# Performance work log

Measured on AMD Instinct MI355X. Metric: run time of the kernel, lower is better.

The kernel has to match this reference:

```python
import jax, jax.numpy as jnp
import numpy as np

L = 2        # NUM_DECODER_LAYERS
D = 512      # D_MODEL == ENCODER_EMBEDDING_DIM == DECODER_EMBEDDING_DIM == DECODER_HIDDEN_DIM
T = 32       # max_trg_len (greedy decode steps)
SOS = 1      # SPECIAL_TOKENS.index('[SOS]'), PAD assumed 0


def setup_inputs() -> dict:
    key = jax.random.key(0)
    ks = jax.random.split(key, 12)
    Vin, Vout, B, S = 32000, 32000, 32, 512
    s = 0.02
    src = jax.random.randint(ks[0], (B, S), 0, Vin)
    src_emb_table = jax.random.normal(ks[1], (Vin, D), dtype=jnp.float32) * s
    trg_emb_table = (jax.random.normal(ks[2], (Vout, D), dtype=jnp.float32) * s).at[0].set(0.0)  # padding_idx=0
    Wih = jax.random.normal(ks[3], (L, 4 * D, D), dtype=jnp.float32) * s
    Whh = jax.random.normal(ks[4], (L, 4 * D, D), dtype=jnp.float32) * s
    bih = jnp.zeros((L, 4 * D), jnp.float32)
    bhh = jnp.zeros((L, 4 * D), jnp.float32)
    Wfc = jax.random.normal(ks[5], (D, D), dtype=jnp.float32) * s      # Decoder.fc_out (hid_dim -> hid_dim)
    bfc = jnp.zeros((D,), jnp.float32)
    Wh2o = jax.random.normal(ks[6], (D, 2 * D), dtype=jnp.float32) * s  # hidden_to_out
    bh2o = jnp.zeros((D,), jnp.float32)
    bout = jnp.zeros((Vout,), jnp.float32)                              # out_layer bias (weight tied to trg_emb_table)
    return dict(src=src, src_emb_table=src_emb_table, trg_emb_table=trg_emb_table,
                Wih=Wih, Whh=Whh, bih=bih, bhh=bhh, Wfc=Wfc, bfc=bfc,
                Wh2o=Wh2o, bh2o=bh2o, bout=bout)


def reference(src, src_emb_table, trg_emb_table, Wih, Whh, bih, bhh, Wfc, bfc, Wh2o, bh2o, bout):
    B, S = src.shape
    dtype = src_emb_table.dtype
    scale = jnp.asarray(D ** 0.5, dtype)
    src_e = src_emb_table[src]  # [B,S,D] -- encoder LSTM hidden/cell are computed but discarded in the original

    def lstm_cell(x, h, c, l):
        g = x @ Wih[l].T + bih[l] + h @ Whh[l].T + bhh[l]
        i, f, gg, o = jnp.split(g, 4, axis=-1)  # torch gate order i,f,g,o
        c2 = jax.nn.sigmoid(f) * c + jax.nn.sigmoid(i) * jnp.tanh(gg)
        h2 = jax.nn.sigmoid(o) * jnp.tanh(c2)
        return h2, c2

    def outer_step(carry, t):
        # Original re-runs the decoder LSTM over the whole generated prefix every
        # step, starting from the carried hidden state; we mask positions > t.
        tokens, h, c = carry  # tokens [B,T+1] int32, h/c [L,B,D]
        emb = jnp.swapaxes(trg_emb_table[tokens[:, :T]], 0, 1)  # [T,B,D]

        def pos_step(hc, inp):
            h, c = hc
            x, pos = inp
            active = pos <= t
            hs, cs = [], []
            for l in range(L):
                h2, c2 = lstm_cell(x, h[l], c[l], l)
                h2 = jnp.where(active, h2, h[l])
                c2 = jnp.where(active, c2, c[l])
                hs.append(h2); cs.append(c2)
                x = h2
            h, c = jnp.stack(hs), jnp.stack(cs)
            return (h, c), h[-1]

        (h, c), h_top = jax.lax.scan(pos_step, (h, c), (emb, jnp.arange(T)))
        out_seq = h_top @ Wfc.T + bfc                 # [T,B,D] Decoder.fc_out
        out_t = jnp.take(out_seq, t, axis=0)          # last valid position (concat[:, -1])
        w = jax.nn.softmax(jnp.einsum('bd,bsd->bs', out_t, src_e) / scale, axis=-1)
        context = jnp.einsum('bs,bsd->bd', w, src_e)
        hid = jax.nn.relu(jnp.concatenate([out_t, context], axis=-1) @ Wh2o.T + bh2o)
        logits = hid @ trg_emb_table.T + bout         # out_layer tied to decoder embedding
        nxt = jnp.argmax(logits, axis=-1).astype(tokens.dtype)
        tokens = tokens.at[:, t + 1].set(nxt)
        return (tokens, h, c), out_seq

    tokens0 = jnp.zeros((B, T + 1), jnp.int32).at[:, 0].set(SOS)
    h0 = jnp.zeros((L, B, D), dtype)
    (tokens, _, _), out_seqs = jax.lax.scan(outer_step, (tokens0, h0, h0), jnp.arange(T))
    # attn returned by the original is from the LAST decode step, queries = all T positions
    attn = jax.nn.softmax(jnp.einsum('tbd,bsd->bts', out_seqs[-1], src_e) / scale, axis=-1)  # [B,T,S]
    return tokens[:, 1:], attn
```

## Files before the change

### kernel.cpp

```cpp
#include <hip/hip_runtime.h>
#include <math.h>

#define NWG 256
#define TPB 512
#define AGT __HIP_MEMORY_SCOPE_AGENT

static constexpr int Bb = 32, Dd = 512, Tt = 32, Vv = 32000;
static constexpr int BD = Bb * Dd;
static constexpr float SCALE_INV = 0.04419417382415922f;

static constexpr size_t OFF_H0 = 8192;
static constexpr size_t OFF_H1 = OFF_H0 + 2 * (size_t)BD;
static constexpr size_t OFF_P  = OFF_H1 + 2 * (size_t)BD;
static constexpr size_t OFF_HL = OFF_P + (size_t)Tt * Bb * 2048;
static constexpr size_t OFF_HD = OFF_HL + (size_t)Tt * BD;
static constexpr size_t OFF_OF = OFF_HD + BD;
static constexpr size_t OFF_CV = OFF_OF + (size_t)Tt * BD;
static constexpr size_t OFF_CI = OFF_CV + 32 * 256;
static constexpr size_t OFF_ET = OFF_CI + 32 * 256;

static constexpr int L_W   = 0;
static constexpr int L_ST  = 13824;
static constexpr int L_SC  = 13824;
static constexpr int L_RB  = 14336;
static constexpr int L_IB  = 15360;
static constexpr int L_RED = 15872;
static constexpr int L_HB  = 30208;
static constexpr int L_GV  = 32256;
static constexpr int L_GI  = 32512;
static constexpr int L_TOK = 32768;
static constexpr int LDS_FLOATS = 32800;
static constexpr size_t LDS_BYTES = (size_t)LDS_FLOATS * 4;

__device__ __forceinline__ float sigm(float x) { return 1.0f / (1.0f + expf(-x)); }

__device__ __forceinline__ float ldcv(const float* p) {
  unsigned u = __hip_atomic_load((const unsigned*)p, __ATOMIC_RELAXED, AGT);
  return __builtin_bit_cast(float, u);
}
__device__ __forceinline__ void stcv(float* p, float v) {
  __hip_atomic_store((unsigned*)p, __builtin_bit_cast(unsigned, v), __ATOMIC_RELAXED, AGT);
}
__device__ __forceinline__ float2 ldcv2(const float* p) {
  unsigned long long u = __hip_atomic_load((const unsigned long long*)p, __ATOMIC_RELAXED, AGT);
  return __builtin_bit_cast(float2, u);
}
__device__ __forceinline__ void stcv2(float* p, float2 v) {
  __hip_atomic_store((unsigned long long*)p, __builtin_bit_cast(unsigned long long, v),
                     __ATOMIC_RELAXED, AGT);
}
__device__ __forceinline__ int ldcvi(const int* p) {
  return (int)__hip_atomic_load((const unsigned*)p, __ATOMIC_RELAXED, AGT);
}
__device__ __forceinline__ void stcvi(int* p, int v) {
  __hip_atomic_store((unsigned*)p, (unsigned)v, __ATOMIC_RELAXED, AGT);
}

__device__ __forceinline__ float wredsum(float v) {
#pragma unroll
  for (int off = 32; off > 0; off >>= 1) v += __shfl_xor(v, off, 64);
  return v;
}

__device__ __forceinline__ float rowReduce16(float x) {
  int t;
  t = __builtin_amdgcn_update_dpp(0, __builtin_bit_cast(int, x), 0x121, 0xF, 0xF, false);
  x += __builtin_bit_cast(float, t);
  t = __builtin_amdgcn_update_dpp(0, __builtin_bit_cast(int, x), 0x122, 0xF, 0xF, false);
  x += __builtin_bit_cast(float, t);
  t = __builtin_amdgcn_update_dpp(0, __builtin_bit_cast(int, x), 0x124, 0xF, 0xF, false);
  x += __builtin_bit_cast(float, t);
  t = __builtin_amdgcn_update_dpp(0, __builtin_bit_cast(int, x), 0x128, 0xF, 0xF, false);
  x += __builtin_bit_cast(float, t);
  return x;
}

__device__ __forceinline__ int swzH(int byte) { return byte ^ (((byte >> 8) & 7) << 4); }

__device__ __forceinline__ void gbar(unsigned* sb, unsigned& lg) {
  const unsigned tgt = lg + 1u;
  asm volatile("s_waitcnt vmcnt(0)" ::: "memory");
  __syncthreads();
  const int wg = (int)blockIdx.x;
  if (threadIdx.x < 64) {
    const int lane = (int)threadIdx.x;
    if (lane == 0)
      __hip_atomic_store(&sb[wg * 16], tgt, __ATOMIC_RELAXED, AGT);
    const int g = wg >> 5;
    if ((wg & 31) == 0) {
      if (lane < 32) {
        const unsigned* slot = &sb[(g * 32 + lane) * 16];
        while (__hip_atomic_load(slot, __ATOMIC_RELAXED, AGT) < tgt)
          __builtin_amdgcn_s_sleep(1);
      }
      if (lane == 0)
        __hip_atomic_store(&sb[4096 + g * 16], tgt, __ATOMIC_RELAXED, AGT);
    }
    if (lane < 8) {
      const unsigned* f = &sb[4096 + lane * 16];
      while (__hip_atomic_load(f, __ATOMIC_RELAXED, AGT) < tgt)
        __builtin_amdgcn_s_sleep(1);
    }
  }
  lg = tgt;
  __syncthreads();
}

__device__ __forceinline__ float blockMax(float v, float* red, int tid) {
#pragma unroll
  for (int off = 32; off > 0; off >>= 1) v = fmaxf(v, __shfl_xor(v, off, 64));
  if ((tid & 63) == 0) red[tid >> 6] = v;
  __syncthreads();
  float m = red[0];
#pragma unroll
  for (int i = 1; i < 8; ++i) m = fmaxf(m, red[i]);
  __syncthreads();
  return m;
}

__device__ __forceinline__ float blockSum(float v, float* red, int tid) {
  v = wredsum(v);
  if ((tid & 63) == 0) red[tid >> 6] = v;
  __syncthreads();
  float s = 0.f;
#pragma unroll
  for (int i = 0; i < 8; ++i) s += red[i];
  __syncthreads();
  return s;
}

__device__ void stageW(int wg, int tid, const float* __restrict__ Wih,
                       const float* __restrict__ Whh, float* __restrict__ SMW) {
  for (int e = tid; e < 24 * 512; e += TPB) {
    const int k = e & 511, rr = e >> 9;
    const int m = rr >> 3, q = (rr >> 1) & 3, dl = rr & 1;
    const int j = q * 512 + wg * 2 + dl;
    const float* srcp = (m == 0) ? (Whh + (size_t)j * 512)
                     : (m == 1) ? (Wih + (size_t)2048 * 512 + (size_t)j * 512)
                                : (Whh + (size_t)2048 * 512 + (size_t)j * 512);
    SMW[rr * 576 + (k >> 5) * 36 + (k & 31)] = srcp[k];
  }
  __syncthreads();
}

__device__ void buildETb(int wg, int tid, const float* __restrict__ Etrg,
                         float* __restrict__ ETb, float* __restrict__ SM) {
  if (wg < 250) {
    for (int tile = 0; tile < 8; ++tile) {
      const int tv = tile >> 2, tk = tile & 3;
      __syncthreads();
      for (int e = tid; e < 64 * 128; e += TPB) {
        const int vl = e >> 7, kl = e & 127;
        SM[vl * 129 + kl] = Etrg[(size_t)(wg * 128 + tv * 64 + vl) * 512 + tk * 128 + kl];
      }
      __syncthreads();
      for (int e = tid; e < 32 * 128; e += TPB) {
        const int vp = e >> 7, kl = e & 127;
        const int v = wg * 128 + tv * 64 + vp * 2;
        const int k = tk * 128 + kl;
        float2 val = make_float2(SM[(vp * 2) * 129 + kl], SM[(vp * 2 + 1) * 129 + kl]);
        stcv2(ETb + ((size_t)(v >> 1) * 512 + k) * 2, val);
      }
    }
    __syncthreads();
  }
}

__device__ __forceinline__ void dotMQ(const float* __restrict__ SMW, int rr, int kc,
                                      const float4* __restrict__ hq, float2& acc) {
  const float4* wr = (const float4*)(SMW + rr * 576 + kc * 36);
#pragma unroll
  for (int i2 = 0; i2 < 8; ++i2) {
    const float4 wv = wr[i2];
    const float4 hA = hq[i2 * 2], hB = hq[i2 * 2 + 1];
    acc.x = fmaf(wv.x, hA.x, acc.x); acc.y = fmaf(wv.x, hA.y, acc.y);
    acc.x = fmaf(wv.y, hA.z, acc.x); acc.y = fmaf(wv.y, hA.w, acc.y);
    acc.x = fmaf(wv.z, hB.x, acc.x); acc.y = fmaf(wv.z, hB.y, acc.y);
    acc.x = fmaf(wv.w, hB.z, acc.x); acc.y = fmaf(wv.w, hB.w, acc.y);
  }
}

__device__ __forceinline__ void phaseAB(
    int wg, int tid, bool doA, bool doB,
    const float* __restrict__ H0r, float* __restrict__ H0w,
    const float* __restrict__ H1r, float* __restrict__ H1w,
    float* __restrict__ HlP, const float* __restrict__ Pp,
    const float* __restrict__ bs1v,
    const float* __restrict__ SMW, float* __restrict__ LH, float* c0, float* c1)
{
  const int b2 = tid >> 5, dl = (tid >> 4) & 1, kc = tid & 15;
  char* LHc = (char*)LH;
  float4 s0[8], s1[8];
  __builtin_amdgcn_sched_barrier(0);
  {
    const float* p0 = H0r + tid * 4;
#pragma unroll
    for (int r = 0; r < 8; ++r)
      asm volatile("global_load_dwordx4 %0, %1, off sc1" : "=v"(s0[r]) : "v"(p0 + r * 2048));
  }
  if (doB) {
    const float* p1 = H1r + tid * 4;
#pragma unroll
    for (int r = 0; r < 8; ++r)
      asm volatile("global_load_dwordx4 %0, %1, off sc1" : "=v"(s1[r]) : "v"(p1 + r * 2048));
    asm volatile("s_waitcnt vmcnt(8)" ::: "memory");
  } else {
    asm volatile("s_waitcnt vmcnt(0)" ::: "memory");
  }
  __builtin_amdgcn_sched_barrier(0);
#pragma unroll
  for (int r = 0; r < 8; ++r)
    *(float4*)(LHc + swzH((r * 512 + tid) * 16)) = s0[r];
  __syncthreads();
  float4 hq[16];
#pragma unroll
  for (int i = 0; i < 16; ++i)
    hq[i] = *(const float4*)(LHc + swzH(b2 * 4096 + kc * 256 + i * 16));

  float2 acc2[12];
#pragma unroll
  for (int j = 0; j < 12; ++j) acc2[j] = make_float2(0.f, 0.f);

  if (doA) {
#pragma unroll
    for (int q = 0; q < 4; ++q) dotMQ(SMW, q * 2 + dl, kc, hq, acc2[q]);
  }
  if (doB) {
#pragma unroll
    for (int q = 0; q < 4; ++q) dotMQ(SMW, 8 + q * 2 + dl, kc, hq, acc2[4 + q]);
    asm volatile("s_waitcnt vmcnt(0)" ::: "memory");
    __builtin_amdgcn_sched_barrier(0);
    __syncthreads();
#pragma unroll
    for (int r = 0; r < 8; ++r)
      *(float4*)(LHc + swzH((r * 512 + tid) * 16)) = s1[r];
    __syncthreads();
#pragma unroll
    for (int i = 0; i < 16; ++i)
      hq[i] = *(const float4*)(LHc + swzH(b2 * 4096 + kc * 256 + i * 16));
#pragma unroll
    for (int q = 0; q < 4; ++q) dotMQ(SMW, 16 + q * 2 + dl, kc, hq, acc2[8 + q]);
  }

#pragma unroll
  for (int j = 0; j < 12; ++j) {
    if (j < 4 ? !doA : !doB) continue;
    acc2[j].x = rowReduce16(acc2[j].x);
    acc2[j].y = rowReduce16(acc2[j].y);
  }

  if (kc == 0) {
    const int d = (wg << 1) | dl;
    if (doA) {
#pragma unroll
      for (int p = 0; p < 2; ++p) {
        const int b = b2 * 2 + p;
        const float* pb = Pp + b * 2048 + d;
        const float gi = (p ? acc2[0].y : acc2[0].x) + pb[0];
        const float gf = (p ? acc2[1].y : acc2[1].x) + pb[512];
        const float gg = (p ? acc2[2].y : acc2[2].x) + pb[1024];
        const float go = (p ? acc2[3].y : acc2[3].x) + pb[1536];
        c0[p] = sigm(gf) * c0[p] + sigm(gi) * tanhf(gg);
        stcv(H0w + b2 * 1024 + d * 2 + p, sigm(go) * tanhf(c0[p]));
      }
    }
    if (doB) {
#pragma unroll
      for (int p = 0; p < 2; ++p) {
        const float gi = (p ? acc2[4].y : acc2[4].x) + (p ? acc2[8].y  : acc2[8].x)  + bs1v[0];
        const float gf = (p ? acc2[5].y : acc2[5].x) + (p ? acc2[9].y  : acc2[9].x)  + bs1v[1];
        const float gg = (p ? acc2[6].y : acc2[6].x) + (p ? acc2[10].y : acc2[10].x) + bs1v[2];
        const float go = (p ? acc2[7].y : acc2[7].x) + (p ? acc2[11].y : acc2[11].x) + bs1v[3];
        c1[p] = sigm(gf) * c1[p] + sigm(gi) * tanhf(gg);
        const float hn = sigm(go) * tanhf(c1[p]);
        stcv(H1w + b2 * 1024 + d * 2 + p, hn);
        if (HlP) stcv(HlP + b2 * 1024 + d * 2 + p, hn);
      }
    }
  }
}

__device__ void phaseCDEF(int b, int tid, const float* __restrict__ H1c,
                          const float* __restrict__ Wfc, const float* __restrict__ bfc,
                          const int* __restrict__ src, const float* __restrict__ Esrc,
                          const float* __restrict__ Wh2o, const float* __restrict__ bh2o,
                          float* __restrict__ hD, float* sc, float* rb, int* ib, float* red)
{
  rb[tid] = ldcv(H1c + (b >> 1) * 1024 + tid * 2 + (b & 1));
  ib[tid] = src[b * 512 + tid];
  __syncthreads();
  const int w = tid >> 6, lane = tid & 63;
  for (int d = w; d < 512; d += 8) {
    const float* wr = Wfc + (size_t)d * 512;
    float p = 0.f;
#pragma unroll
    for (int i = 0; i < 8; ++i) p = fmaf(rb[lane * 8 + i], wr[lane * 8 + i], p);
    p = wredsum(p);
    if (lane == 0) rb[512 + d] = p + bfc[d];
  }
  __syncthreads();
  for (int s = w; s < 512; s += 8) {
    const float* er = Esrc + (size_t)ib[s] * 512;
    float p = 0.f;
#pragma unroll
    for (int i = 0; i < 8; ++i) p = fmaf(rb[512 + lane * 8 + i], er[lane * 8 + i], p);
    p = wredsum(p);
    if (lane == 0) sc[s] = p * SCALE_INV;
  }
  __syncthreads();
  const float mx = blockMax(sc[tid], red, tid);
  const float e = expf(sc[tid] - mx);
  sc[tid] = e;
  const float sum = blockSum(e, red, tid);
  const float inv = 1.0f / sum;
  float acc = 0.f;
#pragma unroll 4
  for (int s = 0; s < 512; ++s) acc = fmaf(sc[s], Esrc[(size_t)ib[s] * 512 + tid], acc);
  rb[tid] = acc * inv;
  __syncthreads();
  for (int d = w; d < 512; d += 8) {
    const float* wr = Wh2o + (size_t)d * 1024;
    float p = 0.f;
#pragma unroll
    for (int i = 0; i < 8; ++i) p = fmaf(rb[512 + lane * 8 + i], wr[lane * 8 + i], p);
#pragma unroll
    for (int i = 0; i < 8; ++i) p = fmaf(rb[lane * 8 + i], wr[512 + lane * 8 + i], p);
    p = wredsum(p);
    if (lane == 0) stcv(hD + (size_t)b * 512 + d, fmaxf(p + bh2o[d], 0.f));
  }
}

__device__ void phaseG(int wg, int tid, int chunk, float* __restrict__ accG,
                       const float* __restrict__ hD, const float* __restrict__ ETb,
                       const float* __restrict__ bout, float* __restrict__ candV,
                       int* __restrict__ candI, float* __restrict__ hblk,
                       float* __restrict__ gv, int* __restrict__ gi)
{
  if (wg >= 250) return;
  if (chunk == 0) {
#pragma unroll
    for (int j = 0; j < 8; ++j) accG[j] = 0.f;
  }
  const int vp = tid >> 3, bh = tid & 7;
  const int v = wg * 128 + vp * 2;
  const float* ep = ETb + (size_t)(v >> 1) * 1024 + chunk * 512;
  const int fk = tid & 63, fb0 = tid >> 6;
  char* hb = (char*)hblk;

  for (int blk = 0; blk < 4; ++blk) {
    const int kb = chunk * 256 + blk * 64;
    __syncthreads();
#pragma unroll
    for (int i = 0; i < 4; ++i) {
      const int b = fb0 + i * 8;
      const float hv = ldcv(hD + (size_t)b * 512 + kb + fk);
      const int byte = fk * 128 + (((b >> 2) * 16) ^ ((fk & 7) << 4)) + ((b & 3) << 2);
      *(float*)(hb + byte) = hv;
    }
    __syncthreads();
#pragma unroll 8
    for (int kk = 0; kk < 64; kk += 2) {
      const float4 e4 = *(const float4*)ep; ep += 4;
      const float4 ha = *(const float4*)(hb + kk * 128 + ((bh * 16) ^ ((kk & 7) << 4)));
      const float4 hbv = *(const float4*)(hb + (kk + 1) * 128 + ((bh * 16) ^ (((kk + 1) & 7) << 4)));
      accG[0] = fmaf(e4.x, ha.x, accG[0]);  accG[4] = fmaf(e4.y, ha.x, accG[4]);
      accG[1] = fmaf(e4.x, ha.y, accG[1]);  accG[5] = fmaf(e4.y, ha.y, accG[5]);
      accG[2] = fmaf(e4.x, ha.z, accG[2]);  accG[6] = fmaf(e4.y, ha.z, accG[6]);
      accG[3] = fmaf(e4.x, ha.w, accG[3]);  accG[7] = fmaf(e4.y, ha.w, accG[7]);
      accG[0] = fmaf(e4.z, hbv.x, accG[0]); accG[4] = fmaf(e4.w, hbv.x, accG[4]);
      accG[1] = fmaf(e4.z, hbv.y, accG[1]); accG[5] = fmaf(e4.w, hbv.y, accG[5]);
      accG[2] = fmaf(e4.z, hbv.z, accG[2]); accG[6] = fmaf(e4.w, hbv.z, accG[6]);
      accG[3] = fmaf(e4.z, hbv.w, accG[3]); accG[7] = fmaf(e4.w, hbv.w, accG[7]);
    }
  }

  if (chunk == 1) {
    const float bo0 = bout[v], bo1 = bout[v + 1];
    const int w = tid >> 6;
#pragma unroll
    for (int j = 0; j < 4; ++j) {
      const float va = accG[j] + bo0, vb = accG[4 + j] + bo1;
      float bv; int bi;
      if (vb > va) { bv = vb; bi = v + 1; } else { bv = va; bi = v; }
#pragma unroll
      for (int off = 8; off < 64; off <<= 1) {
        const float ov = __shfl_xor(bv, off, 64); const int oi = __shfl_xor(bi, off, 64);
        if (ov > bv || (ov == bv && oi < bi)) { bv = ov; bi = oi; }
      }
      if ((tid & 63) < 8) {
        gv[(bh * 4 + j) * 8 + w] = bv;
        gi[(bh * 4 + j) * 8 + w] = bi;
      }
    }
    __syncthreads();
    if (tid < 32) {
      float bv = -INFINITY; int bi = 0;
      for (int w2 = 0; w2 < 8; ++w2) {
        const float vv = gv[tid * 8 + w2]; const int ii = gi[tid * 8 + w2];
        if (vv > bv || (vv == bv && ii < bi)) { bv = vv; bi = ii; }
      }
      stcv(candV + (size_t)tid * 256 + wg, bv);
      stcvi(candI + tid * 256 + wg, bi);
    }
    __syncthreads();
  }
}

__device__ void phaseG_noET(int wg, int tid, const float* __restrict__ hD,
                            const float* __restrict__ Etrg, const float* __restrict__ bout,
                            float* __restrict__ candV, int* __restrict__ candI,
                            float* rb, float* gv, int* gi)
{
  const int b = wg >> 3, vb = wg & 7;
  rb[tid] = ldcv(hD + (size_t)b * 512 + tid);
  __syncthreads();
  const int w = tid >> 6, lane = tid & 63;
  float bv = -INFINITY; int bi = 0;
  for (int v = vb * 4000 + w; v < (vb + 1) * 4000; v += 8) {
    const float* er = Etrg + (size_t)v * 512;
    float p = 0.f;
#pragma unroll
    for (int i = 0; i < 8; ++i) p = fmaf(rb[lane * 8 + i], er[lane * 8 + i], p);
    p = wredsum(p);
    p += bout[v];
    if (p > bv || (p == bv && v < bi)) { bv = p; bi = v; }
  }
  if (lane == 0) { gv[w] = bv; gi[w] = bi; }
  __syncthreads();
  if (tid == 0) {
    float fv = -INFINITY; int fi = 0;
    for (int w2 = 0; w2 < 8; ++w2)
      if (gv[w2] > fv || (gv[w2] == fv && gi[w2] < fi)) { fv = gv[w2]; fi = gi[w2]; }
    stcv(candV + (size_t)b * 256 + vb, fv);
    stcvi(candI + b * 256 + vb, fi);
  }
  __syncthreads();
}

__device__ void phaseHP(int wg, int tid, int t, bool useET,
                        const float* __restrict__ candV, const int* __restrict__ candI,
                        const float* __restrict__ Etrg, const float* __restrict__ Wih,
                        const float* __restrict__ bih, const float* __restrict__ bhh,
                        float* __restrict__ P, float* __restrict__ out, int* tokL)
{
  const int nslot = useET ? 250 : 8;
  {
    const int b = tid >> 4, sl = tid & 15;
    float bv = -INFINITY; int bi = 0x7fffffff;
    for (int s = sl; s < nslot; s += 16) {
      const float vv = ldcv(candV + (size_t)b * 256 + s);
      const int ii = ldcvi(candI + b * 256 + s);
      if (vv > bv || (vv == bv && ii < bi)) { bv = vv; bi = ii; }
    }
#pragma unroll
    for (int off = 1; off < 16; off <<= 1) {
      const float ov = __shfl_xor(bv, off, 64); const int oi = __shfl_xor(bi, off, 64);
      if (ov > bv || (ov == bv && oi < bi)) { bv = ov; bi = oi; }
    }
    if (sl == 0) {
      tokL[b] = bi;
      if (wg == 0) stcv(out + b * 32 + t, (float)bi);
    }
  }
  __syncthreads();
  if (t < 31) {
    const int w = tid >> 6, lane = tid & 63;
    const int q = w >> 1, dl = w & 1;
    const int j = q * 512 + wg * 2 + dl;
    const float* wr = Wih + (size_t)j * 512;
    const float bsum = bih[j] + bhh[j];
    for (int b = 0; b < 32; ++b) {
      const float* er = Etrg + (size_t)tokL[b] * 512;
      float p = 0.f;
#pragma unroll
      for (int i = 0; i < 8; ++i) p = fmaf(er[lane * 8 + i], wr[lane * 8 + i], p);
      p = wredsum(p);
      if (lane == 0) stcv(P + ((size_t)(t + 1) * 32 + b) * 2048 + j, p + bsum);
    }
  }
  __syncthreads();
}

__device__ void phaseX(int wg, int tid, const float* __restrict__ Hl, const float* __restrict__ Wfc,
                       const float* __restrict__ bfc, float* __restrict__ oF)
{
  const int p = wg >> 3, bq = wg & 7;
  const int w = tid >> 6, lane = tid & 63;
  for (int u = w; u < 1024; u += 8) {
    const int b2 = bq * 2 + (u >> 9), d = u & 511;
    const float* hr = Hl + (size_t)p * BD + b2 * 1024;
    const float* wr = Wfc + (size_t)d * 512;
    float ax = 0.f, ay = 0.f;
#pragma unroll
    for (int i = 0; i < 8; ++i) {
      const float2 hv = ldcv2(hr + (lane * 8 + i) * 2);
      const float wv = wr[lane * 8 + i];
      ax = fmaf(hv.x, wv, ax);
      ay = fmaf(hv.y, wv, ay);
    }
    ax = wredsum(ax); ay = wredsum(ay);
    if (lane == 0) {
      stcv(oF + ((size_t)p * 32 + b2 * 2    ) * 512 + d, ax + bfc[d]);
      stcv(oF + ((size_t)p * 32 + b2 * 2 + 1) * 512 + d, ay + bfc[d]);
    }
  }
}

__device__ void phaseY(int wg, int tid, const float* __restrict__ oF, const int* __restrict__ src,
                       const float* __restrict__ Esrc, float* __restrict__ out,
                       float* sc, float* rb, int* ib, float* red)
{
  for (int r = 0; r < 4; ++r) {
    const int id = wg * 4 + r;
    const int b = id >> 5, p = id & 31;
    __syncthreads();
    rb[tid] = ldcv(oF + ((size_t)p * 32 + b) * 512 + tid);
    ib[tid] = src[b * 512 + tid];
    __syncthreads();
    const int w = tid >> 6, lane = tid & 63;
    for (int s = w; s < 512; s += 8) {
      const float* er = Esrc + (size_t)ib[s] * 512;
      float acc = 0.f;
#pragma unroll
      for (int i = 0; i < 8; ++i) acc = fmaf(rb[lane * 8 + i], er[lane * 8 + i], acc);
      acc = wredsum(acc);
      if (lane == 0) sc[s] = acc * SCALE_INV;
    }
    __syncthreads();
    const float mx = blockMax(sc[tid], red, tid);
    const float e = expf(sc[tid] - mx);
    const float sum = blockSum(e, red, tid);
    out[1024 + ((size_t)b * 32 + p) * 512 + tid] = e / sum;
  }
}

extern "C" __global__ void __launch_bounds__(TPB)
s2s_mega(const int* __restrict__ src, const float* __restrict__ Esrc, const float* __restrict__ Etrg,
         const float* __restrict__ Wih, const float* __restrict__ Whh,
         const float* __restrict__ bih, const float* __restrict__ bhh,
         const float* __restrict__ Wfc, const float* __restrict__ bfc,
         const float* __restrict__ Wh2o, const float* __restrict__ bh2o,
         const float* __restrict__ bout, float* __restrict__ out,
         float* __restrict__ ws, const float* __restrict__ ET, float* __restrict__ ETw)
{
  extern __shared__ float SM[];
  float* SMW = SM + L_W;
  float* LH  = SM + L_ST;
  float* sc  = SM + L_SC;
  float* rb  = SM + L_RB;
  int*   ib  = (int*)(SM + L_IB);
  float* red = SM + L_RED;
  float* hblk = SM + L_HB;
  float* gv  = SM + L_GV;
  int*   gi  = (int*)(SM + L_GI);
  int*   tokL = (int*)(SM + L_TOK);

  unsigned* sb = (unsigned*)ws;
  float* H0 = ws + OFF_H0;
  float* H1 = ws + OFF_H1;
  float* P  = ws + OFF_P;
  float* Hl = ws + OFF_HL;
  float* hD = ws + OFF_HD;
  float* oF = ws + OFF_OF;
  float* cV = ws + OFF_CV;
  int*   cI = (int*)(ws + OFF_CI);

  const int wg = blockIdx.x, tid = threadIdx.x;
  const bool useET = (ET != nullptr);
  unsigned lg = 0u;
  float c0[2] = {0.f, 0.f}, c1[2] = {0.f, 0.f};
  float accG[8];

  float bs1v[4];
  {
    const int dl = (tid >> 4) & 1;
    const int d = (wg << 1) | dl;
#pragma unroll
    for (int q = 0; q < 4; ++q)
      bs1v[q] = bih[2048 + q * 512 + d] + bhh[2048 + q * 512 + d];
  }

  {
    const int gid = wg * TPB + tid;
    if (gid < BD) stcv(H0 + gid, 0.f);
    else if (gid < 2 * BD) stcv(H1 + gid - BD, 0.f);
  }
  {
    const int w = tid >> 6, lane = tid & 63;
    const int q = w >> 1, dl = w & 1;
    const int j = q * 512 + wg * 2 + dl;
    const float* er = Etrg + 512;
    const float* wr = Wih + (size_t)j * 512;
    float p = 0.f;
#pragma unroll
    for (int i = 0; i < 8; ++i) p = fmaf(er[lane * 8 + i], wr[lane * 8 + i], p);
    p = wredsum(p);
    p += bih[j] + bhh[j];
    if (lane < 32) stcv(P + (size_t)lane * 2048 + j, p);
  }
  if (ETw) buildETb(wg, tid, Etrg, ETw, LH);
  stageW(wg, tid, Wih, Whh, SMW);
  gbar(sb, lg);

  int cur0 = 0, cur1 = 0;
  for (int t = 0; t < 32; ++t) {
    for (int k = 0; k <= t + 1; ++k) {
      const bool doA = (k <= t), doB = (k >= 1);
      float* HlP = (t == 31 && doB) ? (Hl + (size_t)(k - 1) * BD) : nullptr;
      const int kp = (k < 32) ? k : 31;
      phaseAB(wg, tid, doA, doB,
              H0 + (size_t)cur0 * BD, H0 + (size_t)(cur0 ^ 1) * BD,
              H1 + (size_t)cur1 * BD, H1 + (size_t)(cur1 ^ 1) * BD,
              HlP, P + (size_t)kp * Bb * 2048, bs1v, SMW, LH, c0, c1);
      if (useET) {
        if (t >= 2 && k == 0) {
          phaseG(wg, tid, 0, accG, hD, ET, bout, cV, cI, hblk, gv, gi);
          if (t == 2) phaseG(wg, tid, 1, accG, hD, ET, bout, cV, cI, hblk, gv, gi);
        }
        if (t >= 3 && k == 1)
          phaseG(wg, tid, 1, accG, hD, ET, bout, cV, cI, hblk, gv, gi);
        if (t == 2 && k == 1)
          phaseHP(wg, tid, 1, true, cV, cI, Etrg, Wih, bih, bhh, P, out, tokL);
        if (t >= 3 && k == 2)
          phaseHP(wg, tid, t - 1, true, cV, cI, Etrg, Wih, bih, bhh, P, out, tokL);
      } else {
        if (t >= 2 && k == 0)
          phaseG_noET(wg, tid, hD, Etrg, bout, cV, cI, hblk, gv, gi);
        if (t >= 2 && k == 1)
          phaseHP(wg, tid, t - 1, false, cV, cI, Etrg, Wih, bih, bhh, P, out, tokL);
      }
      gbar(sb, lg);
      if (doA) cur0 ^= 1;
      if (doB) cur1 ^= 1;
    }
    if (wg < 32) phaseCDEF(wg, tid, H1 + (size_t)cur1 * BD, Wfc, bfc, src, Esrc,
                           Wh2o, bh2o, hD, sc, rb, ib, red);
    gbar(sb, lg);
    if (t == 0) {
      if (useET) {
        phaseG(wg, tid, 0, accG, hD, ET, bout, cV, cI, hblk, gv, gi);
        phaseG(wg, tid, 1, accG, hD, ET, bout, cV, cI, hblk, gv, gi);
      } else {
        phaseG_noET(wg, tid, hD, Etrg, bout, cV, cI, hblk, gv, gi);
      }
      gbar(sb, lg);
      phaseHP(wg, tid, 0, useET, cV, cI, Etrg, Wih, bih, bhh, P, out, tokL);
      gbar(sb, lg);
    }
  }
  phaseX(wg, tid, Hl, Wfc, bfc, oF);
  if (useET) {
    phaseG(wg, tid, 0, accG, hD, ET, bout, cV, cI, hblk, gv, gi);
    phaseG(wg, tid, 1, accG, hD, ET, bout, cV, cI, hblk, gv, gi);
  } else {
    phaseG_noET(wg, tid, hD, Etrg, bout, cV, cI, hblk, gv, gi);
  }
  gbar(sb, lg);
  phaseHP(wg, tid, 31, useET, cV, cI, Etrg, Wih, bih, bhh, P, out, tokL);
  phaseY(wg, tid, oF, src, Esrc, out, sc, rb, ib, red);
}

extern "C" void kernel_launch(void* const* d_in, const int* in_sizes, int n_in,
                              void* d_out, int out_size, void* d_ws, size_t ws_size,
                              hipStream_t stream) {
  const int*   src  = (const int*)d_in[0];
  const float* Esrc = (const float*)d_in[1];
  const float* Etrg = (const float*)d_in[2];
  const float* Wih  = (const float*)d_in[3];
  const float* Whh  = (const float*)d_in[4];
  const float* bih  = (const float*)d_in[5];
  const float* bhh  = (const float*)d_in[6];
  const float* Wfc  = (const float*)d_in[7];
  const float* bfc  = (const float*)d_in[8];
  const float* Wh2o = (const float*)d_in[9];
  const float* bh2o = (const float*)d_in[10];
  const float* bout = (const float*)d_in[11];
  float* ws = (float*)d_ws;

  const size_t needET = (OFF_ET + (size_t)512 * 32000) * sizeof(float);
  const bool useET = (ws_size >= needET);
  float* etw = useET ? (ws + OFF_ET) : nullptr;

  (void)hipMemsetAsync(d_ws, 0, 32768, stream);

  (void)hipFuncSetAttribute(reinterpret_cast<const void*>(&s2s_mega),
                            hipFuncAttributeMaxDynamicSharedMemorySize, (int)LDS_BYTES);

  s2s_mega<<<dim3(NWG), dim3(TPB), LDS_BYTES, stream>>>(
      src, Esrc, Etrg, Wih, Whh, bih, bhh, Wfc, bfc, Wh2o, bh2o, bout,
      (float*)d_out, ws, etw, etw);
}
```

Baseline: 18.09 ms.

## Fold attention phase into the LSTM sweep and stagger H loads per workgroup

Measured after the change: 18.02 ms. About the same (-0.3%).

```diff
diff --git a/kernel.cpp b/kernel.cpp
--- a/kernel.cpp
+++ b/kernel.cpp
@@ -189,28 +189,35 @@
     const float* __restrict__ SMW, float* __restrict__ LH, float* c0, float* c1)
 {
   const int b2 = tid >> 5, dl = (tid >> 4) & 1, kc = tid & 15;
+  const int rot = wg & 7;
   char* LHc = (char*)LH;
   float4 s0[8], s1[8];
   __builtin_amdgcn_sched_barrier(0);
   {
     const float* p0 = H0r + tid * 4;
 #pragma unroll
-    for (int r = 0; r < 8; ++r)
-      asm volatile("global_load_dwordx4 %0, %1, off sc1" : "=v"(s0[r]) : "v"(p0 + r * 2048));
+    for (int r = 0; r < 8; ++r) {
+      const int rr = (r + rot) & 7;
+      asm volatile("global_load_dwordx4 %0, %1, off sc1" : "=v"(s0[r]) : "v"(p0 + rr * 2048));
+    }
   }
   if (doB) {
     const float* p1 = H1r + tid * 4;
 #pragma unroll
-    for (int r = 0; r < 8; ++r)
-      asm volatile("global_load_dwordx4 %0, %1, off sc1" : "=v"(s1[r]) : "v"(p1 + r * 2048));
+    for (int r = 0; r < 8; ++r) {
+      const int rr = (r + rot) & 7;
+      asm volatile("global_load_dwordx4 %0, %1, off sc1" : "=v"(s1[r]) : "v"(p1 + rr * 2048));
+    }
     asm volatile("s_waitcnt vmcnt(8)" ::: "memory");
   } else {
     asm volatile("s_waitcnt vmcnt(0)" ::: "memory");
   }
   __builtin_amdgcn_sched_barrier(0);
 #pragma unroll
-  for (int r = 0; r < 8; ++r)
-    *(float4*)(LHc + swzH((r * 512 + tid) * 16)) = s0[r];
+  for (int r = 0; r < 8; ++r) {
+    const int rr = (r + rot) & 7;
+    *(float4*)(LHc + swzH((rr * 512 + tid) * 16)) = s0[r];
+  }
   __syncthreads();
   float4 hq[16];
 #pragma unroll
@@ -232,8 +239,10 @@
     __builtin_amdgcn_sched_barrier(0);
     __syncthreads();
 #pragma unroll
-    for (int r = 0; r < 8; ++r)
-      *(float4*)(LHc + swzH((r * 512 + tid) * 16)) = s1[r];
+    for (int r = 0; r < 8; ++r) {
+      const int rr = (r + rot) & 7;
+      *(float4*)(LHc + swzH((rr * 512 + tid) * 16)) = s1[r];
+    }
     __syncthreads();
 #pragma unroll
     for (int i = 0; i < 16; ++i)
@@ -328,6 +337,7 @@
     p = wredsum(p);
     if (lane == 0) stcv(hD + (size_t)b * 512 + d, fmaxf(p + bh2o[d], 0.f));
   }
+  __syncthreads();
 }
 
 __device__ void phaseG(int wg, int tid, int chunk, float* __restrict__ accG,
@@ -613,16 +623,24 @@
               H1 + (size_t)cur1 * BD, H1 + (size_t)(cur1 ^ 1) * BD,
               HlP, P + (size_t)kp * Bb * 2048, bs1v, SMW, LH, c0, c1);
       if (useET) {
-        if (t >= 2 && k == 0) {
-          phaseG(wg, tid, 0, accG, hD, ET, bout, cV, cI, hblk, gv, gi);
-          if (t == 2) phaseG(wg, tid, 1, accG, hD, ET, bout, cV, cI, hblk, gv, gi);
+        if (t >= 4) {
+          if (k == 0 && wg < 32)
+            phaseCDEF(wg, tid, H1 + (size_t)cur1 * BD, Wfc, bfc, src, Esrc,
+                      Wh2o, bh2o, hD, sc, rb, ib, red);
+          if (k == 1) phaseG(wg, tid, 0, accG, hD, ET, bout, cV, cI, hblk, gv, gi);
+          if (k == 2) phaseG(wg, tid, 1, accG, hD, ET, bout, cV, cI, hblk, gv, gi);
+          if (k == 3) phaseHP(wg, tid, t - 1, true, cV, cI, Etrg, Wih, bih, bhh, P, out, tokL);
+        } else if (t == 3) {
+          if (k == 0) phaseG(wg, tid, 0, accG, hD, ET, bout, cV, cI, hblk, gv, gi);
+          if (k == 1) phaseG(wg, tid, 1, accG, hD, ET, bout, cV, cI, hblk, gv, gi);
+          if (k == 2) phaseHP(wg, tid, 2, true, cV, cI, Etrg, Wih, bih, bhh, P, out, tokL);
+        } else if (t == 2) {
+          if (k == 0) {
+            phaseG(wg, tid, 0, accG, hD, ET, bout, cV, cI, hblk, gv, gi);
+            phaseG(wg, tid, 1, accG, hD, ET, bout, cV, cI, hblk, gv, gi);
+          }
+          if (k == 1) phaseHP(wg, tid, 1, true, cV, cI, Etrg, Wih, bih, bhh, P, out, tokL);
         }
-        if (t >= 3 && k == 1)
-          phaseG(wg, tid, 1, accG, hD, ET, bout, cV, cI, hblk, gv, gi);
-        if (t == 2 && k == 1)
-          phaseHP(wg, tid, 1, true, cV, cI, Etrg, Wih, bih, bhh, P, out, tokL);
-        if (t >= 3 && k == 2)
-          phaseHP(wg, tid, t - 1, true, cV, cI, Etrg, Wih, bih, bhh, P, out, tokL);
       } else {
         if (t >= 2 && k == 0)
           phaseG_noET(wg, tid, hD, Etrg, bout, cV, cI, hblk, gv, gi);
@@ -633,9 +651,11 @@
       if (doA) cur0 ^= 1;
       if (doB) cur1 ^= 1;
     }
-    if (wg < 32) phaseCDEF(wg, tid, H1 + (size_t)cur1 * BD, Wfc, bfc, src, Esrc,
-                           Wh2o, bh2o, hD, sc, rb, ib, red);
-    gbar(sb, lg);
+    if (!useET || t <= 2 || t == 31) {
+      if (wg < 32) phaseCDEF(wg, tid, H1 + (size_t)cur1 * BD, Wfc, bfc, src, Esrc,
+                             Wh2o, bh2o, hD, sc, rb, ib, red);
+      gbar(sb, lg);
+    }
     if (t == 0) {
       if (useET) {
         phaseG(wg, tid, 0, accG, hD, ET, bout, cV, cI, hblk, gv, gi);
```
